# Kernel tuning notes

Measured on AMD Instinct MI355X. Metric: run time of the kernel, lower is better.

## Reference

```python
import jax, jax.numpy as jnp
import numpy as np


def setup_inputs() -> dict:
    key = jax.random.key(0)
    ks = jax.random.split(key, 8)
    B, De, Do, T, H, W = 4, 128, 512, 4, 30, 52
    s = 0.05  # weight init scale
    return {
        "m_in": jax.random.normal(ks[0], (B, De, T, H, W), jnp.float32),
        "m_out": jax.random.normal(ks[1], (B, Do, T, H, W), jnp.float32),
        "q_in": jax.random.normal(ks[2], (B, De, H, W), jnp.float32),
        "q_out": jax.random.normal(ks[3], (B, Do, H, W), jnp.float32),
        "wr": jax.random.normal(ks[4], (Do, 2 * Do), jnp.float32) * s,
        "br": jnp.zeros((Do,), jnp.float32),
        "wu": jax.random.normal(ks[5], (Do, 2 * Do), jnp.float32) * s,
        "bu": jnp.zeros((Do,), jnp.float32),
        "wc": jax.random.normal(ks[6], (Do, 2 * Do), jnp.float32) * s,
        "bc": jnp.zeros((Do,), jnp.float32),
    }


def reference(m_in, m_out, q_in, q_out, wr, br, wu, bu, wc, bc):
    B, De, T, H, W = m_in.shape
    Do = m_out.shape[1]
    PROP_LAYERS = 5

    # --- memory read: pairwise frame attention (bmm + softmax + bmm) ---
    # keys: all T memory frames flattened; queries: current frame.
    mi = m_in.reshape(B, De, T * H * W)            # [B, De, THW]
    qi = q_in.reshape(B, De, H * W)                # [B, De, HW]
    p = jnp.einsum('bdk,bdq->bkq', mi, qi) / (De ** 0.5)  # [B, THW, HW]
    p = jax.nn.softmax(p, axis=1)                  # softmax over memory locations (dim=1 in torch)
    mem = jnp.einsum('bok,bkq->boq', m_out.reshape(B, Do, T * H * W), p)
    mem = mem.reshape(B, Do, H, W)                 # mem_mean; identical every propagate layer

    # --- ConvGRU_h (kernel_size=1 => per-pixel linear gates) ---
    def conv1x1(w, b, x):
        return jnp.einsum('oc,bchw->bohw', w, x) + b[None, :, None, None]

    def gru(x, h):
        xh = jnp.concatenate([x, h], axis=1)                       # [B, 2*Do, H, W]
        r = jax.nn.sigmoid(conv1x1(wr, br, xh))
        u = jax.nn.sigmoid(conv1x1(wu, bu, xh))
        c = jnp.tanh(conv1x1(wc, bc, jnp.concatenate([x, r * h], axis=1)))
        return h * (1.0 - u) + u * c

    q0 = q_out
    q = q_out
    for _ in range(PROP_LAYERS):
        q = gru(q, mem)  # original: q_out = ConvGRU_h(q_out, mem_mean)
    return jnp.concatenate([q, q0], axis=1)  # [B, 2*Do, H, W]
```

## Files before the change

kernel.cpp:

```cpp
#include <hip/hip_runtime.h>
#include <hip/hip_bf16.h>
#include <math.h>

typedef unsigned short u16;
typedef __attribute__((ext_vector_type(8))) short bf16x8;
typedef __attribute__((ext_vector_type(4))) float f32x4;

__device__ __forceinline__ u16 f2bf(float f) {
  union { float f; unsigned u; } x; x.f = f;
  unsigned r = x.u + 0x7fffu + ((x.u >> 16) & 1u);
  return (u16)(r >> 16);
}
__device__ __forceinline__ float bf2f(u16 h) {
  union { unsigned u; float f; } x; x.u = ((unsigned)h) << 16;
  return x.f;
}
__device__ __forceinline__ float sigmf(float x) {
  x = fminf(fmaxf(x, -30.f), 30.f);
  return 1.f / (1.f + __expf(-x));
}
__device__ __forceinline__ float tanh_fast(float x) {
  x = fminf(fmaxf(x, -15.f), 15.f);
  float t = __expf(2.f * x);
  return (t - 1.f) / (t + 1.f);
}

template<int N> __device__ __forceinline__ void wait_vmcnt() {
  if constexpr (N == 0)      asm volatile("s_waitcnt vmcnt(0)" ::: "memory");
  else if constexpr (N == 4) asm volatile("s_waitcnt vmcnt(4)" ::: "memory");
  else if constexpr (N == 6) asm volatile("s_waitcnt vmcnt(6)" ::: "memory");
  else if constexpr (N == 8) asm volatile("s_waitcnt vmcnt(8)" ::: "memory");
  else static_assert(N == 0 || N == 4 || N == 6 || N == 8, "add vmcnt case");
}

#define NB 4
#define DE 128
#define DO_ 512
#define HW 1560
#define THW 6240
#define NP 1664
#define KP 6272
#define PROP 5
#define PVSPLIT 7
#define PVKC 896

template<int MODE, int BMT, int BKT>
__device__ __forceinline__
void gemm_core(const u16* __restrict__ A, const u16* __restrict__ Bt,
               int K, int lda, int ldb, long a_bs, long b_bs,
               void* __restrict__ out0v, long o0_bs, int ld0,
               u16* __restrict__ out1, long o1_bs, int ld1,
               u16* __restrict__ out2, long o2_bs,
               const void* __restrict__ e0v, long e0_bs,
               const void* __restrict__ e1v, long e1_bs,
               const void* __restrict__ e2v, long e2_bs,
               const void* __restrict__ e3v, long e3_bs,
               int nvalid, float scale)
{
  constexpr int WR = BMT / 64;
  constexpr int WC = 4 / WR;
  constexpr int NF = 8 / WC;
  constexpr int KK = BKT / 32;
  constexpr int ASLOT = BMT * BKT / 8;
  constexpr int BSLOT = 128 * BKT / 8;
  constexpr int NISS = (ASLOT + BSLOT) / 256;
  constexpr int RSH = (BMT == 128) ? 7 : 6;
  __shared__ u16 lds[2][ASLOT + BSLOT][8];

  const int tid = threadIdx.x;
  const int wave = tid >> 6, lane = tid & 63;
  const int kg = lane >> 4, lr = lane & 15;
  const int wrw = wave / WC, wcw = wave % WC;
  const long b = blockIdx.z;
  const int m0 = blockIdx.x * BMT, n0 = blockIdx.y * 128;
  A += b * a_bs; Bt += b * b_bs;

  float* out0f = (float*)out0v;
  u16* out0h = (u16*)out0v;
  const float* e0f = (const float*)e0v;
  const u16* e0h = (const u16*)e0v;
  const u16* e1h = (const u16*)e1v;
  const u16* e2h = (const u16*)e2v;
  const u16* e3h = (const u16*)e3v;

  auto stage = [&](int buf, int kt) {
#pragma unroll
    for (int i = 0; i < NISS; ++i) {
      int s = tid + 256 * i;
      const u16* src;
      if (s < ASLOT) {
        int row = s & (BMT - 1), g = s >> RSH;
        src = A + (long)(m0 + row) * lda + kt + g * 8;
      } else {
        int s2 = s - ASLOT;
        int row = s2 & 127, g = s2 >> 7;
        src = Bt + (long)(n0 + row) * ldb + kt + g * 8;
      }
      __builtin_amdgcn_global_load_lds(
          (const __attribute__((address_space(1))) void*)src,
          (__attribute__((address_space(3))) void*)&lds[buf][wave * 64 + 256 * i][0],
          16, 0, 0);
    }
  };

  f32x4 acc[4][NF];
#pragma unroll
  for (int m = 0; m < 4; ++m)
#pragma unroll
    for (int n = 0; n < NF; ++n) acc[m][n] = (f32x4){0.f, 0.f, 0.f, 0.f};

  const int nt = K / BKT;
  stage(0, 0);
  for (int t = 0; t < nt; ++t) {
    int cur = t & 1;
    if (t + 1 < nt) {
      stage(cur ^ 1, (t + 1) * BKT);
      wait_vmcnt<NISS>();
    } else {
      wait_vmcnt<0>();
    }
    __builtin_amdgcn_s_barrier();
    bf16x8 af[KK][4], bfr[KK][NF];
#pragma unroll
    for (int kk = 0; kk < KK; ++kk) {
#pragma unroll
      for (int m = 0; m < 4; ++m)
        af[kk][m] = *(const bf16x8*)&lds[cur][(kk * 4 + kg) * BMT + wrw * 64 + m * 16 + lr][0];
#pragma unroll
      for (int n = 0; n < NF; ++n)
        bfr[kk][n] = *(const bf16x8*)&lds[cur][ASLOT + (kk * 4 + kg) * 128 + (wcw * NF + n) * 16 + lr][0];
    }
#pragma unroll
    for (int kk = 0; kk < KK; ++kk)
#pragma unroll
      for (int m = 0; m < 4; ++m)
#pragma unroll
        for (int n = 0; n < NF; ++n)
          acc[m][n] = __builtin_amdgcn_mfma_f32_16x16x32_bf16(af[kk][m], bfr[kk][n], acc[m][n], 0, 0, 0);
    __builtin_amdgcn_s_barrier();
  }

  if constexpr (MODE == 0) {
    float rs[4][4];
#pragma unroll
    for (int m = 0; m < 4; ++m)
#pragma unroll
      for (int j = 0; j < 4; ++j) rs[m][j] = 0.f;
#pragma unroll
    for (int m = 0; m < 4; ++m) {
      int rloc = wrw * 64 + m * 16 + kg * 4;
#pragma unroll
      for (int n = 0; n < NF; ++n) {
        int col = n0 + (wcw * NF + n) * 16 + lr;
#pragma unroll
        for (int j = 0; j < 4; ++j) {
          long row = m0 + rloc + j;
          float p = __expf(acc[m][n][j] * scale);
          bool valid = (col < nvalid);
          out1[b * o1_bs + row * ld1 + col] = valid ? f2bf(p) : (u16)0;
          rs[m][j] += valid ? p : 0.f;
        }
      }
    }
#pragma unroll
    for (int m = 0; m < 4; ++m)
#pragma unroll
      for (int j = 0; j < 4; ++j) {
#pragma unroll
        for (int msk = 1; msk < 16; msk <<= 1)
          rs[m][j] += __shfl_xor(rs[m][j], msk, 64);
      }
    float* zbuf = (float*)lds;
    if (lr == 0) {
#pragma unroll
      for (int m = 0; m < 4; ++m)
#pragma unroll
        for (int j = 0; j < 4; ++j)
          zbuf[wcw * 128 + wrw * 64 + m * 16 + kg * 4 + j] = rs[m][j];
    }
    __syncthreads();
    if (tid < 128)
      out0f[b * o0_bs + (long)blockIdx.y * NP + (m0 + tid)] = zbuf[tid] + zbuf[128 + tid];
    return;
  }

#pragma unroll
  for (int m = 0; m < 4; ++m) {
    int rloc = wrw * 64 + m * 16 + kg * 4;
#pragma unroll
    for (int n = 0; n < NF; ++n) {
      int col = n0 + (wcw * NF + n) * 16 + lr;
#pragma unroll
      for (int j = 0; j < 4; ++j) {
        long row = m0 + rloc + j;
        float v = acc[m][n][j];
        if constexpr (MODE == 2) {
          out1[b * o1_bs + row * ld1 + col] = f2bf(v + e0f[col]);
        } else if constexpr (MODE == 3) {
          if (col < 1024) {
            float gt = sigmf(v + bf2f(e0h[b * e0_bs + row * 1024 + col]));
            if (col < 512)
              out1[b * o1_bs + row * ld1 + 512 + col] =
                  f2bf(gt * bf2f(e1h[b * e1_bs + row * 512 + col]));
            else
              out0h[b * o0_bs + row * ld0 + (col - 512)] = f2bf(gt);
          } else {
            out2[b * o2_bs + row * 512 + (col - 1024)] = f2bf(v);
          }
        } else if constexpr (MODE == 4) {
          float cg = tanh_fast(v + bf2f(e3h[b * e3_bs + row * 512 + col]) + e0f[col]);
          float u = bf2f(e1h[b * e1_bs + row * 512 + col]);
          float mm = bf2f(e2h[b * e2_bs + row * 512 + col]);
          float x = mm * (1.f - u) + u * cg;
          out1[b * o1_bs + row * ld1 + col] = f2bf(x);
          if (out0f && row < nvalid)
            out0f[b * o0_bs + (long)col * ld0 + row] = x;
        }
      }
    }
  }
}

#define GEMM_ARGS                                                              \
  const u16* __restrict__ A, const u16* __restrict__ Bt, int K, int lda,       \
  int ldb, long a_bs, long b_bs, void* __restrict__ out0v, long o0_bs,         \
  int ld0, u16* __restrict__ out1, long o1_bs, int ld1,                        \
  u16* __restrict__ out2, long o2_bs,                                          \
  const void* __restrict__ e0v, long e0_bs, const void* __restrict__ e1v,      \
  long e1_bs, const void* __restrict__ e2v, long e2_bs,                        \
  const void* __restrict__ e3v, long e3_bs, int nvalid, float scale
#define GEMM_PASS A, Bt, K, lda, ldb, a_bs, b_bs, out0v, o0_bs, ld0, out1,     \
  o1_bs, ld1, out2, o2_bs, e0v, e0_bs, e1v, e1_bs, e2v, e2_bs, e3v, e3_bs,     \
  nvalid, scale

__global__ __launch_bounds__(256) void gk_scores(GEMM_ARGS) { gemm_core<0, 128, 32>(GEMM_PASS); }
__global__ __launch_bounds__(256) void gk_chru(GEMM_ARGS)   { gemm_core<2, 64, 64>(GEMM_PASS); }
__global__ __launch_bounds__(256) void gk_gates(GEMM_ARGS)  { gemm_core<3, 128, 64>(GEMM_PASS); }
__global__ __launch_bounds__(256) void gk_cand(GEMM_ARGS)   { gemm_core<4, 64, 64>(GEMM_PASS); }

__global__ __launch_bounds__(256, 3)
void gemm_pv(const u16* __restrict__ Pt, const u16* __restrict__ moutb,
             u16* __restrict__ Ppart)
{
  const int bid = blockIdx.x;
  const int xcd = bid & 7, i = bid >> 3;
  const int s = xcd * 91 + i;
  const int pair = s / 26, mb = s - pair * 26;
  const int b = pair / PVSPLIT, z = pair - b * PVSPLIT;
  const int m0 = mb * 64;
  const int k0 = z * PVKC;

  const u16* A = Pt + (long)b * NP * KP;
  const u16* B0;
  {
    const u16* Bb = moutb + (long)b * DO_ * KP;
    B0 = Bb + (long)((threadIdx.x >> 6) * 128 + (threadIdx.x & 15)) * KP +
         ((threadIdx.x & 63) >> 4) * 8;
  }

  __shared__ u16 lds[2][2048];
  const int tid = threadIdx.x;
  const int wave = tid >> 6, lane = tid & 63;
  const int kg = lane >> 4, lr = lane & 15;

  auto stage = [&](int buf, int kt) {
    int row = tid & 63, g = tid >> 6;
    const u16* src = A + (long)(m0 + row) * KP + kt + g * 8;
    __builtin_amdgcn_global_load_lds(
        (const __attribute__((address_space(1))) void*)src,
        (__attribute__((address_space(3))) void*)&lds[buf][(wave * 64) * 8],
        16, 0, 0);
  };

  f32x4 acc[4][8];
#pragma unroll
  for (int m = 0; m < 4; ++m)
#pragma unroll
    for (int n = 0; n < 8; ++n) acc[m][n] = (f32x4){0.f, 0.f, 0.f, 0.f};

  bf16x8 bra[8], brb[8];
#pragma unroll
  for (int n = 0; n < 8; ++n)
    bra[n] = *(const bf16x8*)&B0[(long)n * 16 * KP + k0];
  stage(0, k0);
  __syncthreads();

#define PV_STEP(BU, BL, T, CUR)                                                  \
  {                                                                              \
    if ((T) + 1 < 28) {                                                          \
      int ktn = k0 + ((T) + 1) * 32;                                             \
      _Pragma("unroll") for (int n = 0; n < 8; ++n)                              \
          BL[n] = *(const bf16x8*)&B0[(long)n * 16 * KP + ktn];                  \
      stage((CUR) ^ 1, ktn);                                                     \
    }                                                                            \
    bf16x8 af[4];                                                                \
    _Pragma("unroll") for (int m = 0; m < 4; ++m)                                \
        af[m] = *(const bf16x8*)&lds[CUR][(kg * 64 + m * 16 + lr) * 8];          \
    _Pragma("unroll") for (int m = 0; m < 4; ++m)                                \
        _Pragma("unroll") for (int n = 0; n < 8; ++n)                            \
            acc[m][n] = __builtin_amdgcn_mfma_f32_16x16x32_bf16(af[m], BU[n],    \
                                                                acc[m][n], 0, 0, 0); \
    __syncthreads();                                                             \
  }

  for (int tp = 0; tp < 14; ++tp) {
    PV_STEP(bra, brb, 2 * tp, 0);
    PV_STEP(brb, bra, 2 * tp + 1, 1);
  }
#undef PV_STEP

  u16* out = Ppart + (long)(b * PVSPLIT + z) * NP * DO_;
#pragma unroll
  for (int m = 0; m < 4; ++m) {
#pragma unroll
    for (int n = 0; n < 8; ++n) {
      int col = wave * 128 + n * 16 + lr;
#pragma unroll
      for (int j = 0; j < 4; ++j) {
        int row = m0 + m * 16 + kg * 4 + j;
        out[(long)row * DO_ + col] = f2bf(acc[m][n][j]);
      }
    }
  }
}

__global__ void k_transpose_cast(const float* __restrict__ in, u16* __restrict__ out,
                                 int R, int C, int Cp, int out_ld,
                                 long in_bs, long out_bs) {
  __shared__ float t[32][33];
  long b = blockIdx.z;
  int c0 = blockIdx.x * 32, r0 = blockIdx.y * 32;
  int tx = threadIdx.x, ty = threadIdx.y;
#pragma unroll
  for (int i = 0; i < 32; i += 8) {
    int r = r0 + ty + i, c = c0 + tx;
    t[ty + i][tx] = (r < R && c < C) ? in[b * in_bs + (long)r * C + c] : 0.f;
  }
  __syncthreads();
#pragma unroll
  for (int i = 0; i < 32; i += 8) {
    int c = c0 + ty + i, r = r0 + tx;
    if (c < Cp && r < R)
      out[b * out_bs + (long)c * out_ld + r] = f2bf(t[tx][ty + i]);
  }
}

__global__ void k_cast_pad4(const float* __restrict__ in, u16* __restrict__ out,
                            int Cin, int Cout, long in_bs, long out_bs) {
  int c4 = (blockIdx.x * 256 + threadIdx.x) * 4;
  int r = blockIdx.y;
  long b = blockIdx.z;
  if (c4 >= Cout) return;
  uint2 o = {0u, 0u};
  if (c4 < Cin) {
    float4 v = *(const float4*)&in[b * in_bs + (long)r * Cin + c4];
    o.x = (unsigned)f2bf(v.x) | ((unsigned)f2bf(v.y) << 16);
    o.y = (unsigned)f2bf(v.z) | ((unsigned)f2bf(v.w) << 16);
  }
  *(uint2*)&out[b * out_bs + (long)r * Cout + c4] = o;
}

__global__ void k_build_w(const float* __restrict__ wr_, const float* __restrict__ wu_,
                          const float* __restrict__ wc_,
                          u16* __restrict__ wruh, u16* __restrict__ wruxc,
                          u16* __restrict__ wch) {
  int k = blockIdx.x * 256 + threadIdx.x;
  int m = blockIdx.y;
  if (k >= 512) return;
  if (m < 1024) {
    const float* src = (m < 512) ? wr_ : wu_;
    wruh[m * 512 + k] = f2bf(src[(m & 511) * 1024 + 512 + k]);
  } else if (m < 2560) {
    int n = m - 1024;
    const float* src = (n < 512) ? wr_ : ((n < 1024) ? wu_ : wc_);
    wruxc[n * 512 + k] = f2bf(src[(n & 511) * 1024 + k]);
  } else {
    int n = m - 2560;
    wch[n * 512 + k] = f2bf(wc_[n * 1024 + 512 + k]);
  }
}

__global__ void k_bias_ru(const float* __restrict__ br_, const float* __restrict__ bu_,
                          float* __restrict__ bias) {
  int i = blockIdx.x * 256 + threadIdx.x;
  if (i < 1024) bias[i] = (i < 512) ? br_[i] : bu_[i - 512];
}

__global__ void k_invz(const float* __restrict__ Zp, float* __restrict__ invZ) {
  int t = blockIdx.x * 256 + threadIdx.x;
  if (t >= NB * NP) return;
  int b = t / NP, q = t - b * NP;
  const float* base = Zp + (long)b * 49 * NP + q;
  float s = 0.f;
#pragma unroll
  for (int nb = 0; nb < 49; ++nb) s += base[(long)nb * NP];
  invZ[t] = 1.f / s;
}

__global__ void k_reduce_mem(const u16* __restrict__ Ppart, const float* __restrict__ invZ,
                             u16* __restrict__ memTb) {
  long t = (long)blockIdx.x * 256 + threadIdx.x;
  const long bs = (long)NP * DO_;
  if (t >= (long)NB * bs / 8) return;
  long flat = t * 8;
  int b = (int)(flat / bs);
  long r = flat - (long)b * bs;
  int q = (int)(r / DO_);
  float s[8];
#pragma unroll
  for (int e = 0; e < 8; ++e) s[e] = 0.f;
#pragma unroll
  for (int z = 0; z < PVSPLIT; ++z) {
    uint4 v = *(const uint4*)&Ppart[(long)(b * PVSPLIT + z) * bs + r];
    s[0] += bf2f((u16)(v.x & 0xffff)); s[1] += bf2f((u16)(v.x >> 16));
    s[2] += bf2f((u16)(v.y & 0xffff)); s[3] += bf2f((u16)(v.y >> 16));
    s[4] += bf2f((u16)(v.z & 0xffff)); s[5] += bf2f((u16)(v.z >> 16));
    s[6] += bf2f((u16)(v.w & 0xffff)); s[7] += bf2f((u16)(v.w >> 16));
  }
  float iz = invZ[b * NP + q];
  uint4 o;
  o.x = (unsigned)f2bf(s[0] * iz) | ((unsigned)f2bf(s[1] * iz) << 16);
  o.y = (unsigned)f2bf(s[2] * iz) | ((unsigned)f2bf(s[3] * iz) << 16);
  o.z = (unsigned)f2bf(s[4] * iz) | ((unsigned)f2bf(s[5] * iz) << 16);
  o.w = (unsigned)f2bf(s[6] * iz) | ((unsigned)f2bf(s[7] * iz) << 16);
  *(uint4*)&memTb[(long)b * bs + r] = o;
}

__global__ void k_copy_q0(const float4* __restrict__ src, float4* __restrict__ dst) {
  int idx = blockIdx.x * 256 + threadIdx.x;
  long b = blockIdx.z;
  const long n4 = (long)DO_ * HW / 4;
  if (idx < n4)
    dst[b * ((long)1024 * HW / 4) + n4 + idx] = src[b * n4 + idx];
}

extern "C" void kernel_launch(void* const* d_in, const int* in_sizes, int n_in,
                              void* d_out, int out_size, void* d_ws, size_t ws_size,
                              hipStream_t stream) {
  const float* m_in  = (const float*)d_in[0];
  const float* m_out = (const float*)d_in[1];
  const float* q_in  = (const float*)d_in[2];
  const float* q_out = (const float*)d_in[3];
  const float* wr    = (const float*)d_in[4];
  const float* br    = (const float*)d_in[5];
  const float* wu    = (const float*)d_in[6];
  const float* bu    = (const float*)d_in[7];
  const float* wc    = (const float*)d_in[8];
  const float* bc    = (const float*)d_in[9];
  float* dout = (float*)d_out;

  char* p = (char*)d_ws;
  size_t off = 0;
  auto alloc = [&](size_t bytes) { void* r = p + off; off += (bytes + 255) & ~(size_t)255; return r; };
  u16*   miT    = (u16*)alloc((size_t)NB * KP * DE * 2);
  u16*   qiT    = (u16*)alloc((size_t)NB * NP * DE * 2);
  u16*   Pt     = (u16*)alloc((size_t)NB * NP * KP * 2);
  float* invZ   = (float*)alloc((size_t)NB * NP * 4);
  u16*   moutb  = (u16*)alloc((size_t)NB * DO_ * KP * 2);
  u16*   memTb  = (u16*)alloc((size_t)NB * NP * DO_ * 2);
  u16*   chru   = (u16*)alloc((size_t)NB * NP * 1024 * 2);
  u16*   U      = (u16*)alloc((size_t)NB * NP * DO_ * 2);
  u16*   XRb    = (u16*)alloc((size_t)NB * NP * 1024 * 2);
  float* Qfin   = (float*)alloc((size_t)NB * NP * DO_ * 4);
  (void)Qfin;
  u16*   XRa    = (u16*)alloc((size_t)NB * NP * 1024 * 2);
  u16*   Cx     = (u16*)alloc((size_t)NB * NP * 512 * 2);
  u16*   wruh   = (u16*)alloc((size_t)1024 * 512 * 2);
  u16*   wruxc  = (u16*)alloc((size_t)1536 * 512 * 2);
  u16*   wch    = (u16*)alloc((size_t)512 * 512 * 2);
  float* biasru = (float*)alloc((size_t)1024 * 4);
  u16*   Ppart  = (u16*)chru;
  float* Zp     = (float*)memTb;
  if (off > ws_size) return;

  k_build_w<<<dim3(2, 3072), 256, 0, stream>>>(wr, wu, wc, wruh, wruxc, wch);
  k_bias_ru<<<dim3(4), 256, 0, stream>>>(br, bu, biasru);
  k_cast_pad4<<<dim3(7, 512, NB), 256, 0, stream>>>(
      m_out, moutb, THW, KP, (long)DO_ * THW, (long)DO_ * KP);
  k_transpose_cast<<<dim3(196, 4, NB), dim3(32, 8), 0, stream>>>(
      m_in, miT, DE, THW, KP, DE, (long)DE * THW, (long)KP * DE);
  k_transpose_cast<<<dim3(52, 4, NB), dim3(32, 8), 0, stream>>>(
      q_in, qiT, DE, HW, NP, DE, (long)DE * HW, (long)NP * DE);
  k_transpose_cast<<<dim3(52, 16, NB), dim3(32, 8), 0, stream>>>(
      q_out, XRa, DO_, HW, NP, 1024, (long)DO_ * HW, (long)NP * 1024);

  gk_scores<<<dim3(13, 49, NB), 256, 0, stream>>>(
      qiT, miT, DE, DE, DE, (long)NP * DE, (long)KP * DE,
      Zp, (long)49 * NP, 0, Pt, (long)NP * KP, KP, nullptr, 0,
      nullptr, 0, nullptr, 0, nullptr, 0, nullptr, 0, THW, 0.08838834764831845f);
  k_invz<<<dim3(26), 256, 0, stream>>>(Zp, invZ);

  gemm_pv<<<dim3(728), 256, 0, stream>>>(Pt, moutb, Ppart);
  k_reduce_mem<<<dim3(1664), 256, 0, stream>>>(Ppart, invZ, memTb);

  gk_chru<<<dim3(26, 8, NB), 256, 0, stream>>>(
      memTb, wruh, DO_, DO_, DO_, (long)NP * DO_, 0,
      nullptr, 0, 0, chru, (long)NP * 1024, 1024, nullptr, 0,
      biasru, 0, nullptr, 0, nullptr, 0, nullptr, 0, 0, 0.f);

  u16* xr[2] = {XRa, XRb};
  for (int l = 0; l < PROP; ++l) {
    u16* cur = xr[l & 1];
    u16* nxt = xr[(l + 1) & 1];
    gk_gates<<<dim3(13, 12, NB), 256, 0, stream>>>(
        cur, wruxc, DO_, 1024, DO_, (long)NP * 1024, 0,
        U, (long)NP * DO_, DO_, cur, (long)NP * 1024, 1024,
        Cx, (long)NP * 512,
        chru, (long)NP * 1024, memTb, (long)NP * DO_, nullptr, 0,
        nullptr, 0, 0, 0.f);
    gk_cand<<<dim3(26, 4, NB), 256, 0, stream>>>(
        cur + 512, wch, DO_, 1024, DO_, (long)NP * 1024, 0,
        (l == PROP - 1) ? (void*)dout : nullptr, (long)1024 * HW, HW,
        nxt, (long)NP * 1024, 1024, nullptr, 0,
        bc, 0, U, (long)NP * DO_, memTb, (long)NP * DO_,
        Cx, (long)NP * 512, HW, 0.f);
  }

  k_copy_q0<<<dim3(780, 1, NB), 256, 0, stream>>>((const float4*)q_out, (float4*)dout);
}
```

Baseline: 726.7 us.

## Load PV GEMM A tiles directly to registers, drop LDS staging and barriers

The PV GEMM kernel now loads its A-operand fragments straight from global memory into registers, double-buffered two k-steps ahead, instead of staging them through LDS with global_load_lds. B-fragment loads are interleaved with the MFMAs per column. This removes the per-step __syncthreads and LDS traffic, and launch bounds drop from 3 to 2 blocks per CU to make room for the extra registers. Each wave now loads its own A rows, with no sharing across waves, so global/L2 traffic for A goes up and occupancy may fall.

```diff
diff --git a/kernel.cpp b/kernel.cpp
--- a/kernel.cpp
+++ b/kernel.cpp
@@ -238,7 +238,7 @@
 __global__ __launch_bounds__(256) void gk_gates(GEMM_ARGS)  { gemm_core<3, 128, 64>(GEMM_PASS); }
 __global__ __launch_bounds__(256) void gk_cand(GEMM_ARGS)   { gemm_core<4, 64, 64>(GEMM_PASS); }
 
-__global__ __launch_bounds__(256, 3)
+__global__ __launch_bounds__(256, 2)
 void gemm_pv(const u16* __restrict__ Pt, const u16* __restrict__ moutb,
              u16* __restrict__ Ppart)
 {
@@ -250,27 +250,12 @@
   const int m0 = mb * 64;
   const int k0 = z * PVKC;
 
-  const u16* A = Pt + (long)b * NP * KP;
-  const u16* B0;
-  {
-    const u16* Bb = moutb + (long)b * DO_ * KP;
-    B0 = Bb + (long)((threadIdx.x >> 6) * 128 + (threadIdx.x & 15)) * KP +
-         ((threadIdx.x & 63) >> 4) * 8;
-  }
-
-  __shared__ u16 lds[2][2048];
   const int tid = threadIdx.x;
   const int wave = tid >> 6, lane = tid & 63;
   const int kg = lane >> 4, lr = lane & 15;
 
-  auto stage = [&](int buf, int kt) {
-    int row = tid & 63, g = tid >> 6;
-    const u16* src = A + (long)(m0 + row) * KP + kt + g * 8;
-    __builtin_amdgcn_global_load_lds(
-        (const __attribute__((address_space(1))) void*)src,
-        (__attribute__((address_space(3))) void*)&lds[buf][(wave * 64) * 8],
-        16, 0, 0);
-  };
+  const u16* A0 = Pt + (long)b * NP * KP + (long)(m0 + lr) * KP + kg * 8 + k0;
+  const u16* B0 = moutb + (long)b * DO_ * KP + (long)(wave * 128 + lr) * KP + kg * 8 + k0;
 
   f32x4 acc[4][8];
 #pragma unroll
@@ -278,35 +263,34 @@
 #pragma unroll
     for (int n = 0; n < 8; ++n) acc[m][n] = (f32x4){0.f, 0.f, 0.f, 0.f};
 
-  bf16x8 bra[8], brb[8];
-#pragma unroll
-  for (int n = 0; n < 8; ++n)
-    bra[n] = *(const bf16x8*)&B0[(long)n * 16 * KP + k0];
-  stage(0, k0);
-  __syncthreads();
-
-#define PV_STEP(BU, BL, T, CUR)                                                  \
+  bf16x8 a0_[4], a1_[4], b_[8];
+#pragma unroll
+  for (int m = 0; m < 4; ++m) a0_[m] = *(const bf16x8*)&A0[(long)m * 16 * KP];
+#pragma unroll
+  for (int n = 0; n < 8; ++n) b_[n] = *(const bf16x8*)&B0[(long)n * 16 * KP];
+#pragma unroll
+  for (int m = 0; m < 4; ++m) a1_[m] = *(const bf16x8*)&A0[(long)m * 16 * KP + 32];
+
+#define PV_STEP(AU, T, LB, LA)                                                   \
   {                                                                              \
-    if ((T) + 1 < 28) {                                                          \
-      int ktn = k0 + ((T) + 1) * 32;                                             \
-      _Pragma("unroll") for (int n = 0; n < 8; ++n)                              \
-          BL[n] = *(const bf16x8*)&B0[(long)n * 16 * KP + ktn];                  \
-      stage((CUR) ^ 1, ktn);                                                     \
+    _Pragma("unroll") for (int n = 0; n < 8; ++n) {                              \
+      _Pragma("unroll") for (int m = 0; m < 4; ++m)                              \
+          acc[m][n] = __builtin_amdgcn_mfma_f32_16x16x32_bf16(AU[m], b_[n],      \
+                                                              acc[m][n], 0, 0, 0); \
+      if (LB) b_[n] = *(const bf16x8*)&B0[(long)n * 16 * KP + ((T) + 1) * 32];   \
     }                                                                            \
-    bf16x8 af[4];                                                                \
-    _Pragma("unroll") for (int m = 0; m < 4; ++m)                                \
-        af[m] = *(const bf16x8*)&lds[CUR][(kg * 64 + m * 16 + lr) * 8];          \
-    _Pragma("unroll") for (int m = 0; m < 4; ++m)                                \
-        _Pragma("unroll") for (int n = 0; n < 8; ++n)                            \
-            acc[m][n] = __builtin_amdgcn_mfma_f32_16x16x32_bf16(af[m], BU[n],    \
-                                                                acc[m][n], 0, 0, 0); \
-    __syncthreads();                                                             \
-  }
-
-  for (int tp = 0; tp < 14; ++tp) {
-    PV_STEP(bra, brb, 2 * tp, 0);
-    PV_STEP(brb, bra, 2 * tp + 1, 1);
-  }
+    if (LA) {                                                                    \
+      _Pragma("unroll") for (int m = 0; m < 4; ++m)                              \
+          AU[m] = *(const bf16x8*)&A0[(long)m * 16 * KP + ((T) + 2) * 32];       \
+    }                                                                            \
+  }
+
+  for (int tp = 0; tp < 13; ++tp) {
+    PV_STEP(a0_, 2 * tp, 1, 1);
+    PV_STEP(a1_, 2 * tp + 1, 1, 1);
+  }
+  PV_STEP(a0_, 26, 1, 0);
+  PV_STEP(a1_, 27, 0, 0);
 #undef PV_STEP
 
   u16* out = Ppart + (long)(b * PVSPLIT + z) * NP * DO_;
```

Result: faster. 679.6 us (-6.5%).
